# Kernel tuning notes

Measured on AMD Instinct MI355X. Metric: run time of the kernel, lower is better.

The kernel has to match this reference:

```python
import jax, jax.numpy as jnp
import numpy as np

N = 100000
E = 1600000
IN_C, HID_C, OUT_C = 128, 64, 64
LAYERS = 2


def setup_inputs() -> dict:
    key = jax.random.key(0)
    ks = jax.random.split(key, 7)
    x = jax.random.normal(ks[0], (N, IN_C), dtype=jnp.float32)
    edge_index = jax.random.randint(ks[1], (2, E), 0, N, dtype=jnp.int32)
    W_init = jax.random.normal(ks[2], (IN_C, HID_C), dtype=jnp.float32) / np.sqrt(IN_C)
    W_self = jax.random.normal(ks[3], (LAYERS, HID_C, HID_C), dtype=jnp.float32) / np.sqrt(HID_C)
    W_agg = jax.random.normal(ks[4], (LAYERS, HID_C, HID_C), dtype=jnp.float32) / np.sqrt(HID_C)
    b = jnp.zeros((LAYERS, HID_C), dtype=jnp.float32)
    W_out = jax.random.normal(ks[5], (HID_C, OUT_C), dtype=jnp.float32) / np.sqrt(HID_C)
    return {"x": x, "edge_index": edge_index, "W_init": W_init,
            "W_self": W_self, "W_agg": W_agg, "b": b, "W_out": W_out}


def reference(x, edge_index, W_init, W_self, W_agg, b, W_out):
    # edge (dst, src): aggregated_neighbors[edge[0]].append(x[edge[1]])
    dst = edge_index[0]
    src = edge_index[1]
    n = x.shape[0]
    # in-degree for mean aggregation (clamp to 1 for isolated nodes)
    deg = jax.ops.segment_sum(jnp.ones((src.shape[0],), dtype=x.dtype), dst,
                              num_segments=n)
    deg = jnp.maximum(deg, 1.0)[:, None]  # [N,1]
    h = x @ W_init  # initialize: [N, hid]
    for l in range(LAYERS):
        msgs = h[src]  # per-edge gather [E, hid]
        agg = jax.ops.segment_sum(msgs, dst, num_segments=n) / deg  # mean aggregate
        h = jax.nn.relu(agg @ W_agg[l] + h @ W_self[l] + b[l])  # combine
    return h @ W_out  # output: [N, out]
```

## Files before the change

### kernel.cpp

```cpp
#include <hip/hip_runtime.h>
#include <hip/hip_fp16.h>

#define N_NODES 100000
#define E_EDGES 1600000
#define IN_C    128
#define HID_C   64
#define OUT_C   64
#define ROWS    32
#define NBUCK   391
#define BSHIFT  8
#define BNODES  256
#define CAP     5120
#define CHUNK   4096

typedef _Float16 f16x8 __attribute__((ext_vector_type(8)));
typedef float    f32x4 __attribute__((ext_vector_type(4)));
#define MFMA16(a, b, c) __builtin_amdgcn_mfma_f32_16x16x32_f16(a, b, c, 0, 0, 0)

__global__ __launch_bounds__(256) void bin_kernel(const int* __restrict__ ei,
                                                  int* __restrict__ bucket_cursor,
                                                  unsigned int* __restrict__ gbuck) {
    __shared__ int hist[NBUCK];
    __shared__ int resbase[NBUCK];
    __shared__ int cur[NBUCK];
    __shared__ unsigned int pk[CHUNK];
    __shared__ unsigned short bk[CHUNK];
    int tid = threadIdx.x;
    for (int i = tid; i < NBUCK; i += 256) hist[i] = 0;
    __syncthreads();
    int base = blockIdx.x * CHUNK;
    for (int i = tid; i < CHUNK; i += 256) {
        int e = base + i;
        if (e < E_EDGES) {
            int dst = ei[e];
            int src = ei[E_EDGES + e];
            int b = dst >> BSHIFT;
            pk[i] = ((unsigned)(dst & (BNODES - 1)) << 17) | (unsigned)src;
            bk[i] = (unsigned short)b;
            atomicAdd(&hist[b], 1);
        } else bk[i] = 0xFFFF;
    }
    __syncthreads();
    for (int i = tid; i < NBUCK; i += 256) {
        resbase[i] = atomicAdd(&bucket_cursor[i], hist[i]);
        cur[i] = 0;
    }
    __syncthreads();
    for (int i = tid; i < CHUNK; i += 256) {
        if (bk[i] != 0xFFFF) {
            int b = bk[i];
            int slot = resbase[b] + atomicAdd(&cur[b], 1);
            if (slot < CAP) gbuck[(size_t)b * CAP + slot] = pk[i];
        }
    }
}

__global__ __launch_bounds__(512) void scan_buckets(const int* __restrict__ bucket_cursor,
                                                    int* __restrict__ bucket_base) {
    __shared__ int s[512];
    int t = threadIdx.x;
    int v = (t < NBUCK) ? min(bucket_cursor[t], CAP) : 0;
    s[t] = v;
    __syncthreads();
    for (int off = 1; off < 512; off <<= 1) {
        int u = (t >= off) ? s[t - off] : 0;
        __syncthreads();
        s[t] += u;
        __syncthreads();
    }
    if (t < NBUCK) bucket_base[t] = s[t] - v;
}

__global__ __launch_bounds__(256) void build_bucket(const unsigned int* __restrict__ gbuck,
                                                    const int* __restrict__ bucket_cursor,
                                                    const int* __restrict__ bucket_base,
                                                    int* __restrict__ csr,
                                                    int2* __restrict__ rc) {
    __shared__ int lcnt[BNODES];
    __shared__ int lpos[BNODES];
    __shared__ int lcur[BNODES];
    __shared__ int ss[256];
    int t = threadIdx.x;
    int b = blockIdx.x;
    int gnode = b * BNODES;
    int nn = min(BNODES, N_NODES - gnode);
    int ec = min(bucket_cursor[b], CAP);
    int bb = bucket_base[b];
    lcnt[t] = 0; lcur[t] = 0;
    __syncthreads();
    const unsigned int* mybuck = gbuck + (size_t)b * CAP;
    for (int i = t; i < ec; i += 256)
        atomicAdd(&lcnt[mybuck[i] >> 17], 1);
    __syncthreads();
    int c = lcnt[t];
    ss[t] = c;
    __syncthreads();
    for (int off = 1; off < 256; off <<= 1) {
        int u = (t >= off) ? ss[t - off] : 0;
        __syncthreads();
        ss[t] += u;
        __syncthreads();
    }
    int ex = ss[t] - c;
    lpos[t] = ex;
    if (t < nn) rc[gnode + t] = make_int2(bb + ex, c);
    __syncthreads();
    for (int i = t; i < ec; i += 256) {
        unsigned int p = mybuck[i];
        int dl = p >> 17;
        int slot = lpos[dl] + atomicAdd(&lcur[dl], 1);
        csr[bb + slot] = (int)(p & 0x1FFFF);
    }
}

__global__ __launch_bounds__(256) void transpose_weights(const float* __restrict__ Wi,
                                                         const float* __restrict__ Wsf,
                                                         const float* __restrict__ Waf,
                                                         const float* __restrict__ Wo,
                                                         _Float16* __restrict__ wtr) {
    int t = blockIdx.x * 256 + threadIdx.x;
    if (t < 8192) {
        int k = t >> 6, col = t & 63;
        wtr[col * 136 + k] = (_Float16)Wi[t];
    } else if (t < 24576) {
        int u = t - 8192; int l = u >> 13; int v = u & 8191;
        int k = v >> 6, col = v & 63;
        float w = (k < 64) ? Waf[l * 4096 + k * 64 + col] : Wsf[l * 4096 + (k - 64) * 64 + col];
        wtr[8704 + l * 8704 + col * 136 + k] = (_Float16)w;
    } else if (t < 28672) {
        int u = t - 24576; int k = u >> 6, col = u & 63;
        wtr[26112 + col * 72 + k] = (_Float16)Wo[u];
    }
}

template<int K>
__device__ __forceinline__ void mfma_tile(const _Float16* sA, const _Float16* sBt,
                                          int lane, int wave, f32x4 acc[2]) {
    const int LDA = K + 8;
    int r0 = (wave >> 1) * 16;
    int wc = wave & 1;
    int m = lane & 15, kg = lane >> 4;
    acc[0] = (f32x4){0.f, 0.f, 0.f, 0.f};
    acc[1] = (f32x4){0.f, 0.f, 0.f, 0.f};
    #pragma unroll
    for (int ks = 0; ks < K / 32; ++ks) {
        f16x8 a = *(const f16x8*)&sA[(r0 + m) * LDA + 32 * ks + 8 * kg];
        #pragma unroll
        for (int nt = 0; nt < 2; ++nt) {
            f16x8 b = *(const f16x8*)&sBt[(wc * 32 + nt * 16 + m) * LDA + 32 * ks + 8 * kg];
            acc[nt] = MFMA16(a, b, acc[nt]);
        }
    }
}

__global__ __launch_bounds__(256) void init_gemm(const float* __restrict__ x,
                                                 const float4* __restrict__ wtrI,
                                                 __half* __restrict__ h) {
    __shared__ _Float16 sA[ROWS][IN_C + 8];
    __shared__ _Float16 sBt[HID_C][IN_C + 8];
    int tid = threadIdx.x;
    float4* sB4 = (float4*)&sBt[0][0];
    for (int i = tid; i < 1088; i += 256) sB4[i] = wtrI[i];
    int row0 = blockIdx.x * ROWS;
    const float4* x4 = (const float4*)x;
    for (int i = tid; i < ROWS * 32; i += 256) {
        int r = i >> 5, q = i & 31;
        float4 f = x4[(size_t)(row0 + r) * 32 + q];
        __half2 ha = __floats2half2_rn(f.x, f.y), hb = __floats2half2_rn(f.z, f.w);
        uint2 u; u.x = *(unsigned*)&ha; u.y = *(unsigned*)&hb;
        *(uint2*)&sA[r][q * 4] = u;
    }
    __syncthreads();
    int lane = tid & 63, wave = tid >> 6;
    f32x4 acc[2];
    mfma_tile<IN_C>(&sA[0][0], &sBt[0][0], lane, wave, acc);
    int m = lane & 15, rg = lane >> 4;
    int r0 = (wave >> 1) * 16, wc = wave & 1;
    #pragma unroll
    for (int nt = 0; nt < 2; ++nt) {
        int col = wc * 32 + nt * 16 + m;
        #pragma unroll
        for (int i = 0; i < 4; ++i) {
            int row = row0 + r0 + rg * 4 + i;
            h[(size_t)row * HID_C + col] = __float2half(acc[nt][i]);
        }
    }
}

template<bool FINAL>
__global__ __launch_bounds__(256) void fused_layer(const __half* __restrict__ h,
                                                   const int2* __restrict__ rc,
                                                   const int* __restrict__ csr,
                                                   const float4* __restrict__ wtrL,
                                                   const float* __restrict__ bias,
                                                   __half* __restrict__ hout,
                                                   const float4* __restrict__ wtrO,
                                                   float* __restrict__ out) {
    __shared__ _Float16 sA[ROWS][136];
    __shared__ _Float16 sBt[HID_C][136];
    int tid = threadIdx.x;
    float4* sB4 = (float4*)&sBt[0][0];
    for (int i = tid; i < 1088; i += 256) sB4[i] = wtrL[i];
    int row0 = blockIdx.x * ROWS;
    int wave = tid >> 6, lane = tid & 63;
    int g4 = lane >> 4;
    int c16 = lane & 15;
    const uint2* h2u = (const uint2*)h;
    const __half2 hzero = __floats2half2_rn(0.f, 0.f);
    for (int i = 0; i < 8; ++i) {
        int rl = wave * 8 + i;
        int row = row0 + rl;
        int2 rcv = rc[row];
        int start = __builtin_amdgcn_readfirstlane(rcv.x);
        int d     = __builtin_amdgcn_readfirstlane(rcv.y);
        uint2 selfv = h2u[(size_t)row * 16 + c16];
        __half2 p01 = hzero, p23 = hzero;
        int j = 0;
        for (; j + 16 <= d; j += 16) {
            uint2 v[4];
            #pragma unroll
            for (int s = 0; s < 4; ++s) {
                int src = csr[start + j + s * 4 + g4];
                v[s] = h2u[(size_t)src * 16 + c16];
            }
            #pragma unroll
            for (int s = 0; s < 4; ++s) {
                p01 += *(__half2*)&v[s].x;
                p23 += *(__half2*)&v[s].y;
            }
        }
        if (j < d) {
            int dm1 = d - 1;
            #pragma unroll
            for (int s = 0; s < 4; ++s) {
                int e = j + s * 4 + g4;
                bool ok = e < d;
                int src = csr[start + min(e, dm1)];
                uint2 vv = h2u[(size_t)src * 16 + c16];
                unsigned vx = ok ? vv.x : 0u, vy = ok ? vv.y : 0u;
                p01 += *(__half2*)&vx;
                p23 += *(__half2*)&vy;
            }
        }
        unsigned u01 = *(unsigned*)&p01, u23 = *(unsigned*)&p23;
        unsigned o01 = (unsigned)__shfl_xor((int)u01, 16), o23 = (unsigned)__shfl_xor((int)u23, 16);
        p01 += *(__half2*)&o01; p23 += *(__half2*)&o23;
        u01 = *(unsigned*)&p01; u23 = *(unsigned*)&p23;
        o01 = (unsigned)__shfl_xor((int)u01, 32); o23 = (unsigned)__shfl_xor((int)u23, 32);
        p01 += *(__half2*)&o01; p23 += *(__half2*)&o23;
        if (lane < 16) {
            __half2 hinv = __float2half2_rn(1.f / fmaxf((float)d, 1.f));
            p01 *= hinv; p23 *= hinv;
            uint2 agg2; agg2.x = *(unsigned*)&p01; agg2.y = *(unsigned*)&p23;
            *(uint2*)&sA[rl][4 * c16]      = agg2;
            *(uint2*)&sA[rl][64 + 4 * c16] = selfv;
        }
    }
    __syncthreads();
    f32x4 acc[2];
    mfma_tile<128>(&sA[0][0], &sBt[0][0], lane, wave, acc);
    int m = lane & 15, rg = lane >> 4;
    int r0 = (wave >> 1) * 16, wc = wave & 1;
    if (!FINAL) {
        #pragma unroll
        for (int nt = 0; nt < 2; ++nt) {
            int col = wc * 32 + nt * 16 + m;
            float bv = bias[col];
            #pragma unroll
            for (int i = 0; i < 4; ++i) {
                int row = row0 + r0 + rg * 4 + i;
                hout[(size_t)row * HID_C + col] = __float2half(fmaxf(acc[nt][i] + bv, 0.f));
            }
        }
    } else {
        __syncthreads();
        _Float16* sA72 = &sA[0][0];
        #pragma unroll
        for (int nt = 0; nt < 2; ++nt) {
            int col = wc * 32 + nt * 16 + m;
            float bv = bias[col];
            #pragma unroll
            for (int i = 0; i < 4; ++i) {
                int rl = r0 + rg * 4 + i;
                sA72[rl * 72 + col] = (_Float16)fmaxf(acc[nt][i] + bv, 0.f);
            }
        }
        for (int i = tid; i < 576; i += 256) sB4[i] = wtrO[i];
        __syncthreads();
        f32x4 acc2[2];
        mfma_tile<64>(&sA[0][0], &sBt[0][0], lane, wave, acc2);
        #pragma unroll
        for (int nt = 0; nt < 2; ++nt) {
            int col = wc * 32 + nt * 16 + m;
            #pragma unroll
            for (int i = 0; i < 4; ++i) {
                int row = row0 + r0 + rg * 4 + i;
                out[(size_t)row * OUT_C + col] = acc2[nt][i];
            }
        }
    }
}

extern "C" void kernel_launch(void* const* d_in, const int* in_sizes, int n_in,
                              void* d_out, int out_size, void* d_ws, size_t ws_size,
                              hipStream_t stream) {
    const float* x      = (const float*)d_in[0];
    const int*   ei     = (const int*)  d_in[1];
    const float* W_init = (const float*)d_in[2];
    const float* W_self = (const float*)d_in[3];
    const float* W_agg  = (const float*)d_in[4];
    const float* b      = (const float*)d_in[5];
    const float* W_out  = (const float*)d_in[6];
    float* out = (float*)d_out;

    char* ws = (char*)d_ws;
    const size_t KB = 1 << 10;
    int*      bucket_cursor = (int*)(ws + 0);
    int*      bucket_base   = (int*)(ws + 2 * KB);
    int2*     rc            = (int2*)(ws + 4 * KB);
    int*      csr           = (int*)(ws + 1024 * KB);
    _Float16* wtr           = (_Float16*)(ws + 7424 * KB);
    unsigned* gbuck         = (unsigned*)(ws + 8192 * KB);
    __half*   hA            = (__half*)(ws + 18432 * KB);
    __half*   hB            = (__half*)(ws + 32768 * KB);

    const float4* wtrI  = (const float4*)(wtr);
    const float4* wtrL0 = (const float4*)(wtr + 8704);
    const float4* wtrL1 = (const float4*)(wtr + 17408);
    const float4* wtrO  = (const float4*)(wtr + 26112);

    transpose_weights<<<112, 256, 0, stream>>>(W_init, W_self, W_agg, W_out, wtr);

    hipMemsetAsync(bucket_cursor, 0, NBUCK * sizeof(int), stream);
    bin_kernel<<<(E_EDGES + CHUNK - 1) / CHUNK, 256, 0, stream>>>(ei, bucket_cursor, gbuck);
    scan_buckets<<<1, 512, 0, stream>>>(bucket_cursor, bucket_base);
    build_bucket<<<NBUCK, 256, 0, stream>>>(gbuck, bucket_cursor, bucket_base, csr, rc);

    const int GB = N_NODES / ROWS;

    init_gemm<<<GB, 256, 0, stream>>>(x, wtrI, hA);

    fused_layer<false><<<GB, 256, 0, stream>>>(hA, rc, csr, wtrL0, b + 0 * HID_C, hB,
                                               wtrO, out);
    fused_layer<true><<<GB, 256, 0, stream>>>(hB, rc, csr, wtrL1, b + 1 * HID_C, hA,
                                              wtrO, out);
}
```

Measured before the change: 168.4 us.

## Merge preprocessing kernels and stage CSR indices in LDS for batched gather

Combines binning with the weight transpose in one launch, and folds the bucket scan into the CSR build, which runs in the same launch as the init GEMM. This cuts six launches to two. The fused layer now preloads each block's CSR index range and self rows into shared memory, then gathers eight rows at once with unrolled chunks to raise memory-level parallelism. Costs are redundant per-block scans, higher register pressure, and a capped index buffer (IDXMAX) that clamps edges for blocks with unusually many edges.

Result: faster. 144.0 us (-14.5%).

```diff
diff --git a/kernel.cpp b/kernel.cpp
--- a/kernel.cpp
+++ b/kernel.cpp
@@ -12,126 +12,78 @@
 #define BNODES  256
 #define CAP     5120
 #define CHUNK   4096
+#define NB_BINCH 391
+#define NB_TR   112
+#define IDXCAP  1632
+#define IDXMAX  1568
 
 typedef _Float16 f16x8 __attribute__((ext_vector_type(8)));
 typedef float    f32x4 __attribute__((ext_vector_type(4)));
 #define MFMA16(a, b, c) __builtin_amdgcn_mfma_f32_16x16x32_f16(a, b, c, 0, 0, 0)
 
-__global__ __launch_bounds__(256) void bin_kernel(const int* __restrict__ ei,
-                                                  int* __restrict__ bucket_cursor,
-                                                  unsigned int* __restrict__ gbuck) {
-    __shared__ int hist[NBUCK];
-    __shared__ int resbase[NBUCK];
-    __shared__ int cur[NBUCK];
-    __shared__ unsigned int pk[CHUNK];
-    __shared__ unsigned short bk[CHUNK];
+struct BinS {
+    int hist[NBUCK]; int resbase[NBUCK]; int cur[NBUCK];
+    unsigned pk[CHUNK]; unsigned short bk[CHUNK];
+};
+
+__global__ __launch_bounds__(256) void k1_bin_tr(const int* __restrict__ ei,
+                                                 int* __restrict__ bucket_cursor,
+                                                 unsigned* __restrict__ gbuck,
+                                                 const float* __restrict__ Wi,
+                                                 const float* __restrict__ Wsf,
+                                                 const float* __restrict__ Waf,
+                                                 const float* __restrict__ Wo,
+                                                 _Float16* __restrict__ wtr) {
+    __shared__ BinS S;
     int tid = threadIdx.x;
-    for (int i = tid; i < NBUCK; i += 256) hist[i] = 0;
-    __syncthreads();
-    int base = blockIdx.x * CHUNK;
-    for (int i = tid; i < CHUNK; i += 256) {
-        int e = base + i;
-        if (e < E_EDGES) {
-            int dst = ei[e];
-            int src = ei[E_EDGES + e];
-            int b = dst >> BSHIFT;
-            pk[i] = ((unsigned)(dst & (BNODES - 1)) << 17) | (unsigned)src;
-            bk[i] = (unsigned short)b;
-            atomicAdd(&hist[b], 1);
-        } else bk[i] = 0xFFFF;
-    }
-    __syncthreads();
-    for (int i = tid; i < NBUCK; i += 256) {
-        resbase[i] = atomicAdd(&bucket_cursor[i], hist[i]);
-        cur[i] = 0;
-    }
-    __syncthreads();
-    for (int i = tid; i < CHUNK; i += 256) {
-        if (bk[i] != 0xFFFF) {
-            int b = bk[i];
-            int slot = resbase[b] + atomicAdd(&cur[b], 1);
-            if (slot < CAP) gbuck[(size_t)b * CAP + slot] = pk[i];
-        }
-    }
-}
-
-__global__ __launch_bounds__(512) void scan_buckets(const int* __restrict__ bucket_cursor,
-                                                    int* __restrict__ bucket_base) {
-    __shared__ int s[512];
-    int t = threadIdx.x;
-    int v = (t < NBUCK) ? min(bucket_cursor[t], CAP) : 0;
-    s[t] = v;
-    __syncthreads();
-    for (int off = 1; off < 512; off <<= 1) {
-        int u = (t >= off) ? s[t - off] : 0;
-        __syncthreads();
-        s[t] += u;
-        __syncthreads();
-    }
-    if (t < NBUCK) bucket_base[t] = s[t] - v;
-}
-
-__global__ __launch_bounds__(256) void build_bucket(const unsigned int* __restrict__ gbuck,
-                                                    const int* __restrict__ bucket_cursor,
-                                                    const int* __restrict__ bucket_base,
-                                                    int* __restrict__ csr,
-                                                    int2* __restrict__ rc) {
-    __shared__ int lcnt[BNODES];
-    __shared__ int lpos[BNODES];
-    __shared__ int lcur[BNODES];
-    __shared__ int ss[256];
-    int t = threadIdx.x;
-    int b = blockIdx.x;
-    int gnode = b * BNODES;
-    int nn = min(BNODES, N_NODES - gnode);
-    int ec = min(bucket_cursor[b], CAP);
-    int bb = bucket_base[b];
-    lcnt[t] = 0; lcur[t] = 0;
-    __syncthreads();
-    const unsigned int* mybuck = gbuck + (size_t)b * CAP;
-    for (int i = t; i < ec; i += 256)
-        atomicAdd(&lcnt[mybuck[i] >> 17], 1);
-    __syncthreads();
-    int c = lcnt[t];
-    ss[t] = c;
-    __syncthreads();
-    for (int off = 1; off < 256; off <<= 1) {
-        int u = (t >= off) ? ss[t - off] : 0;
-        __syncthreads();
-        ss[t] += u;
-        __syncthreads();
-    }
-    int ex = ss[t] - c;
-    lpos[t] = ex;
-    if (t < nn) rc[gnode + t] = make_int2(bb + ex, c);
-    __syncthreads();
-    for (int i = t; i < ec; i += 256) {
-        unsigned int p = mybuck[i];
-        int dl = p >> 17;
-        int slot = lpos[dl] + atomicAdd(&lcur[dl], 1);
-        csr[bb + slot] = (int)(p & 0x1FFFF);
-    }
-}
-
-__global__ __launch_bounds__(256) void transpose_weights(const float* __restrict__ Wi,
-                                                         const float* __restrict__ Wsf,
-                                                         const float* __restrict__ Waf,
-                                                         const float* __restrict__ Wo,
-                                                         _Float16* __restrict__ wtr) {
-    int t = blockIdx.x * 256 + threadIdx.x;
-    if (t < 8192) {
-        int k = t >> 6, col = t & 63;
-        wtr[col * 136 + k] = (_Float16)Wi[t];
-    } else if (t < 24576) {
-        int u = t - 8192; int l = u >> 13; int v = u & 8191;
-        int k = v >> 6, col = v & 63;
-        float w = (k < 64) ? Waf[l * 4096 + k * 64 + col] : Wsf[l * 4096 + (k - 64) * 64 + col];
-        wtr[8704 + l * 8704 + col * 136 + k] = (_Float16)w;
-    } else if (t < 28672) {
-        int u = t - 24576; int k = u >> 6, col = u & 63;
-        wtr[26112 + col * 72 + k] = (_Float16)Wo[u];
-    }
-}
+    if (blockIdx.x < NB_BINCH) {
+        for (int i = tid; i < NBUCK; i += 256) S.hist[i] = 0;
+        __syncthreads();
+        int base = blockIdx.x * CHUNK;
+        for (int i = tid; i < CHUNK; i += 256) {
+            int e = base + i;
+            if (e < E_EDGES) {
+                int dst = ei[e];
+                int src = ei[E_EDGES + e];
+                int b = dst >> BSHIFT;
+                S.pk[i] = ((unsigned)(dst & (BNODES - 1)) << 17) | (unsigned)src;
+                S.bk[i] = (unsigned short)b;
+                atomicAdd(&S.hist[b], 1);
+            } else S.bk[i] = 0xFFFF;
+        }
+        __syncthreads();
+        for (int i = tid; i < NBUCK; i += 256) {
+            S.resbase[i] = atomicAdd(&bucket_cursor[i], S.hist[i]);
+            S.cur[i] = 0;
+        }
+        __syncthreads();
+        for (int i = tid; i < CHUNK; i += 256) {
+            if (S.bk[i] != 0xFFFF) {
+                int b = S.bk[i];
+                int slot = S.resbase[b] + atomicAdd(&S.cur[b], 1);
+                if (slot < CAP) gbuck[(size_t)b * CAP + slot] = S.pk[i];
+            }
+        }
+    } else {
+        int t = (blockIdx.x - NB_BINCH) * 256 + tid;
+        if (t < 8192) {
+            int k = t >> 6, col = t & 63;
+            wtr[col * 136 + k] = (_Float16)Wi[t];
+        } else if (t < 24576) {
+            int u = t - 8192; int l = u >> 13; int v = u & 8191;
+            int k = v >> 6, col = v & 63;
+            float w = (k < 64) ? Waf[l * 4096 + k * 64 + col] : Wsf[l * 4096 + (k - 64) * 64 + col];
+            wtr[8704 + l * 8704 + col * 136 + k] = (_Float16)w;
+        } else if (t < 28672) {
+            int u = t - 24576; int k = u >> 6, col = u & 63;
+            wtr[26112 + col * 72 + k] = (_Float16)Wo[u];
+        }
+    }
+}
+
+struct InitS { _Float16 sA[ROWS][IN_C + 8]; _Float16 sBt[HID_C][IN_C + 8]; };
+struct BuildS { int lcnt[BNODES]; int lpos[BNODES]; int lcur[BNODES]; int s[2][512]; };
+union K2S { InitS ini; BuildS bld; };
 
 template<int K>
 __device__ __forceinline__ void mfma_tile(const _Float16* sA, const _Float16* sBt,
@@ -153,39 +105,105 @@
     }
 }
 
-__global__ __launch_bounds__(256) void init_gemm(const float* __restrict__ x,
-                                                 const float4* __restrict__ wtrI,
-                                                 __half* __restrict__ h) {
-    __shared__ _Float16 sA[ROWS][IN_C + 8];
-    __shared__ _Float16 sBt[HID_C][IN_C + 8];
-    int tid = threadIdx.x;
-    float4* sB4 = (float4*)&sBt[0][0];
-    for (int i = tid; i < 1088; i += 256) sB4[i] = wtrI[i];
-    int row0 = blockIdx.x * ROWS;
-    const float4* x4 = (const float4*)x;
-    for (int i = tid; i < ROWS * 32; i += 256) {
-        int r = i >> 5, q = i & 31;
-        float4 f = x4[(size_t)(row0 + r) * 32 + q];
-        __half2 ha = __floats2half2_rn(f.x, f.y), hb = __floats2half2_rn(f.z, f.w);
-        uint2 u; u.x = *(unsigned*)&ha; u.y = *(unsigned*)&hb;
-        *(uint2*)&sA[r][q * 4] = u;
-    }
-    __syncthreads();
-    int lane = tid & 63, wave = tid >> 6;
-    f32x4 acc[2];
-    mfma_tile<IN_C>(&sA[0][0], &sBt[0][0], lane, wave, acc);
-    int m = lane & 15, rg = lane >> 4;
-    int r0 = (wave >> 1) * 16, wc = wave & 1;
-    #pragma unroll
-    for (int nt = 0; nt < 2; ++nt) {
-        int col = wc * 32 + nt * 16 + m;
-        #pragma unroll
-        for (int i = 0; i < 4; ++i) {
-            int row = row0 + r0 + rg * 4 + i;
-            h[(size_t)row * HID_C + col] = __float2half(acc[nt][i]);
-        }
-    }
-}
+__global__ __launch_bounds__(256) void k2_build_init(const unsigned* __restrict__ gbuck,
+                                                     const int* __restrict__ bucket_cursor,
+                                                     int* __restrict__ csr,
+                                                     int2* __restrict__ rc,
+                                                     const float* __restrict__ x,
+                                                     const float4* __restrict__ wtrI,
+                                                     __half* __restrict__ h) {
+    __shared__ K2S U;
+    int t = threadIdx.x;
+    if (blockIdx.x < NBUCK) {
+        BuildS& S = U.bld;
+        int b = blockIdx.x;
+        int v0 = (t < NBUCK) ? min(bucket_cursor[t], CAP) : 0;
+        int v1 = (t + 256 < NBUCK) ? min(bucket_cursor[t + 256], CAP) : 0;
+        S.s[0][t] = v0; S.s[0][t + 256] = v1;
+        S.lcnt[t] = 0; S.lcur[t] = 0;
+        __syncthreads();
+        int p = 0;
+        for (int off = 1; off < 512; off <<= 1) {
+            int a0 = S.s[p][t]       + ((t >= off)       ? S.s[p][t - off] : 0);
+            int a1 = S.s[p][t + 256] + ((t + 256 >= off) ? S.s[p][t + 256 - off] : 0);
+            S.s[p ^ 1][t] = a0; S.s[p ^ 1][t + 256] = a1;
+            __syncthreads();
+            p ^= 1;
+        }
+        int bb = (b == 0) ? 0 : S.s[p][b - 1];
+        int ec = min(bucket_cursor[b], CAP);
+        int gnode = b * BNODES;
+        int nn = min(BNODES, N_NODES - gnode);
+        const unsigned* mybuck = gbuck + (size_t)b * CAP;
+        __syncthreads();
+        for (int i = t; i < ec; i += 256) atomicAdd(&S.lcnt[mybuck[i] >> 17], 1);
+        __syncthreads();
+        int c = S.lcnt[t];
+        S.s[0][t] = c;
+        __syncthreads();
+        int q = 0;
+        for (int off = 1; off < 256; off <<= 1) {
+            int a0 = S.s[q][t] + ((t >= off) ? S.s[q][t - off] : 0);
+            S.s[q ^ 1][t] = a0;
+            __syncthreads();
+            q ^= 1;
+        }
+        int ex = S.s[q][t] - c;
+        S.lpos[t] = ex;
+        if (t < nn) rc[gnode + t] = make_int2(bb + ex, c);
+        __syncthreads();
+        for (int i = t; i < ec; i += 256) {
+            unsigned pkt = mybuck[i];
+            int dl = pkt >> 17;
+            int slot = S.lpos[dl] + atomicAdd(&S.lcur[dl], 1);
+            csr[bb + slot] = (int)(pkt & 0x1FFFF);
+        }
+    } else {
+        InitS& S = U.ini;
+        int row0 = (blockIdx.x - NBUCK) * ROWS;
+        float4* sB4 = (float4*)&S.sBt[0][0];
+        for (int i = t; i < 1088; i += 256) sB4[i] = wtrI[i];
+        const float4* x4 = (const float4*)x;
+        for (int i = t; i < ROWS * 32; i += 256) {
+            int r = i >> 5, qq = i & 31;
+            float4 f = x4[(size_t)(row0 + r) * 32 + qq];
+            __half2 ha = __floats2half2_rn(f.x, f.y), hb = __floats2half2_rn(f.z, f.w);
+            uint2 u; u.x = *(unsigned*)&ha; u.y = *(unsigned*)&hb;
+            *(uint2*)&S.sA[r][qq * 4] = u;
+        }
+        __syncthreads();
+        int lane = t & 63, wave = t >> 6;
+        f32x4 acc[2];
+        mfma_tile<IN_C>(&S.sA[0][0], &S.sBt[0][0], lane, wave, acc);
+        int m = lane & 15, rg = lane >> 4;
+        int r0 = (wave >> 1) * 16, wc = wave & 1;
+        #pragma unroll
+        for (int nt = 0; nt < 2; ++nt) {
+            int col = wc * 32 + nt * 16 + m;
+            #pragma unroll
+            for (int i = 0; i < 4; ++i) {
+                int row = row0 + r0 + rg * 4 + i;
+                h[(size_t)row * HID_C + col] = __float2half(acc[nt][i]);
+            }
+        }
+    }
+}
+
+#define GCHUNK(r, JB, CLAMP)                                                    \
+    {                                                                           \
+        _Pragma("unroll")                                                       \
+        for (int s = 0; s < 4; ++s) {                                           \
+            int ee = (JB) + s * 4 + g4;                                         \
+            int a = sl[r] + ee;                                                 \
+            if (CLAMP) a = min(a, IDXCAP - 1);                                  \
+            int src = sIdx[a];                                                  \
+            uint2 vv = h2u[(size_t)src * 16 + c16];                             \
+            bool ok = ee < dd[r];                                               \
+            unsigned vx = ok ? vv.x : 0u, vy = ok ? vv.y : 0u;                  \
+            p01[r] += *(__half2*)&vx;                                           \
+            p23[r] += *(__half2*)&vy;                                           \
+        }                                                                       \
+    }
 
 template<bool FINAL>
 __global__ __launch_bounds__(256) void fused_layer(const __half* __restrict__ h,
@@ -198,65 +216,75 @@
                                                    float* __restrict__ out) {
     __shared__ _Float16 sA[ROWS][136];
     __shared__ _Float16 sBt[HID_C][136];
+    __shared__ int sIdx[IDXCAP];
+    __shared__ int2 sRC[ROWS];
     int tid = threadIdx.x;
     float4* sB4 = (float4*)&sBt[0][0];
     for (int i = tid; i < 1088; i += 256) sB4[i] = wtrL[i];
     int row0 = blockIdx.x * ROWS;
+    const uint2* h2u = (const uint2*)h;
+
+    if (tid < 32) sRC[tid] = rc[row0 + tid];
+    int2 rcF = rc[row0];
+    int2 rcL = rc[row0 + 31];
+    int e0 = __builtin_amdgcn_readfirstlane(rcF.x);
+    int e1 = __builtin_amdgcn_readfirstlane(rcL.x) + __builtin_amdgcn_readfirstlane(rcL.y);
+    int Lc = min(e1 - e0, IDXMAX);
+    for (int i = tid; i < Lc; i += 256) sIdx[i] = csr[e0 + i];
+    if (tid < 64) sIdx[min(Lc + tid, IDXCAP - 1)] = 0;
+    for (int i = tid; i < 512; i += 256) {
+        int r = i >> 4, qq = i & 15;
+        *(uint2*)&sA[r][64 + qq * 4] = h2u[(size_t)(row0 + r) * 16 + qq];
+    }
+    __syncthreads();
+
     int wave = tid >> 6, lane = tid & 63;
     int g4 = lane >> 4;
     int c16 = lane & 15;
-    const uint2* h2u = (const uint2*)h;
+    int sl[8], dd[8];
+    #pragma unroll
+    for (int r = 0; r < 8; ++r) {
+        int2 v = sRC[wave * 8 + r];
+        sl[r] = min(__builtin_amdgcn_readfirstlane(v.x) - e0, IDXMAX);
+        dd[r] = __builtin_amdgcn_readfirstlane(v.y);
+    }
     const __half2 hzero = __floats2half2_rn(0.f, 0.f);
-    for (int i = 0; i < 8; ++i) {
-        int rl = wave * 8 + i;
-        int row = row0 + rl;
-        int2 rcv = rc[row];
-        int start = __builtin_amdgcn_readfirstlane(rcv.x);
-        int d     = __builtin_amdgcn_readfirstlane(rcv.y);
-        uint2 selfv = h2u[(size_t)row * 16 + c16];
-        __half2 p01 = hzero, p23 = hzero;
-        int j = 0;
-        for (; j + 16 <= d; j += 16) {
-            uint2 v[4];
-            #pragma unroll
-            for (int s = 0; s < 4; ++s) {
-                int src = csr[start + j + s * 4 + g4];
-                v[s] = h2u[(size_t)src * 16 + c16];
-            }
-            #pragma unroll
-            for (int s = 0; s < 4; ++s) {
-                p01 += *(__half2*)&v[s].x;
-                p23 += *(__half2*)&v[s].y;
-            }
-        }
-        if (j < d) {
-            int dm1 = d - 1;
-            #pragma unroll
-            for (int s = 0; s < 4; ++s) {
-                int e = j + s * 4 + g4;
-                bool ok = e < d;
-                int src = csr[start + min(e, dm1)];
-                uint2 vv = h2u[(size_t)src * 16 + c16];
-                unsigned vx = ok ? vv.x : 0u, vy = ok ? vv.y : 0u;
-                p01 += *(__half2*)&vx;
-                p23 += *(__half2*)&vy;
-            }
-        }
-        unsigned u01 = *(unsigned*)&p01, u23 = *(unsigned*)&p23;
-        unsigned o01 = (unsigned)__shfl_xor((int)u01, 16), o23 = (unsigned)__shfl_xor((int)u23, 16);
-        p01 += *(__half2*)&o01; p23 += *(__half2*)&o23;
-        u01 = *(unsigned*)&p01; u23 = *(unsigned*)&p23;
-        o01 = (unsigned)__shfl_xor((int)u01, 32); o23 = (unsigned)__shfl_xor((int)u23, 32);
-        p01 += *(__half2*)&o01; p23 += *(__half2*)&o23;
+    __half2 p01[8], p23[8];
+    #pragma unroll
+    for (int r = 0; r < 8; ++r) { p01[r] = hzero; p23[r] = hzero; }
+
+    #pragma unroll
+    for (int r = 0; r < 8; ++r) GCHUNK(r, 0, false)
+    #pragma unroll
+    for (int r = 0; r < 8; ++r) GCHUNK(r, 16, false)
+    int dmax = dd[0];
+    #pragma unroll
+    for (int r = 1; r < 8; ++r) dmax = max(dmax, dd[r]);
+    if (dmax > 32) {
+        #pragma unroll
+        for (int r = 0; r < 8; ++r)
+            for (int j = 32; j < dd[r]; j += 16) GCHUNK(r, j, true)
+    }
+
+    #pragma unroll
+    for (int r = 0; r < 8; ++r) {
+        unsigned u01 = *(unsigned*)&p01[r], u23 = *(unsigned*)&p23[r];
+        unsigned o01 = (unsigned)__shfl_xor((int)u01, 16);
+        unsigned o23 = (unsigned)__shfl_xor((int)u23, 16);
+        p01[r] += *(__half2*)&o01; p23[r] += *(__half2*)&o23;
+        u01 = *(unsigned*)&p01[r]; u23 = *(unsigned*)&p23[r];
+        o01 = (unsigned)__shfl_xor((int)u01, 32);
+        o23 = (unsigned)__shfl_xor((int)u23, 32);
+        p01[r] += *(__half2*)&o01; p23[r] += *(__half2*)&o23;
         if (lane < 16) {
-            __half2 hinv = __float2half2_rn(1.f / fmaxf((float)d, 1.f));
-            p01 *= hinv; p23 *= hinv;
-            uint2 agg2; agg2.x = *(unsigned*)&p01; agg2.y = *(unsigned*)&p23;
-            *(uint2*)&sA[rl][4 * c16]      = agg2;
-            *(uint2*)&sA[rl][64 + 4 * c16] = selfv;
+            __half2 hinv = __float2half2_rn(1.f / fmaxf((float)dd[r], 1.f));
+            __half2 q01 = p01[r] * hinv, q23 = p23[r] * hinv;
+            uint2 agg2; agg2.x = *(unsigned*)&q01; agg2.y = *(unsigned*)&q23;
+            *(uint2*)&sA[wave * 8 + r][4 * c16] = agg2;
         }
     }
     __syncthreads();
+
     f32x4 acc[2];
     mfma_tile<128>(&sA[0][0], &sBt[0][0], lane, wave, acc);
     int m = lane & 15, rg = lane >> 4;
@@ -316,7 +344,6 @@
     char* ws = (char*)d_ws;
     const size_t KB = 1 << 10;
     int*      bucket_cursor = (int*)(ws + 0);
-    int*      bucket_base   = (int*)(ws + 2 * KB);
     int2*     rc            = (int2*)(ws + 4 * KB);
     int*      csr           = (int*)(ws + 1024 * KB);
     _Float16* wtr           = (_Float16*)(ws + 7424 * KB);
@@ -329,17 +356,12 @@
     const float4* wtrL1 = (const float4*)(wtr + 17408);
     const float4* wtrO  = (const float4*)(wtr + 26112);
 
-    transpose_weights<<<112, 256, 0, stream>>>(W_init, W_self, W_agg, W_out, wtr);
-
     hipMemsetAsync(bucket_cursor, 0, NBUCK * sizeof(int), stream);
-    bin_kernel<<<(E_EDGES + CHUNK - 1) / CHUNK, 256, 0, stream>>>(ei, bucket_cursor, gbuck);
-    scan_buckets<<<1, 512, 0, stream>>>(bucket_cursor, bucket_base);
-    build_bucket<<<NBUCK, 256, 0, stream>>>(gbuck, bucket_cursor, bucket_base, csr, rc);
-
+    k1_bin_tr<<<NB_BINCH + NB_TR, 256, 0, stream>>>(ei, bucket_cursor, gbuck,
+                                                    W_init, W_self, W_agg, W_out, wtr);
+    k2_build_init<<<NBUCK + N_NODES / ROWS, 256, 0, stream>>>(gbuck, bucket_cursor, csr, rc,
+                                                              x, wtrI, hA);
     const int GB = N_NODES / ROWS;
-
-    init_gemm<<<GB, 256, 0, stream>>>(x, wtrI, hA);
-
     fused_layer<false><<<GB, 256, 0, stream>>>(hA, rc, csr, wtrL0, b + 0 * HID_C, hB,
                                                wtrO, out);
     fused_layer<true><<<GB, 256, 0, stream>>>(hB, rc, csr, wtrL1, b + 1 * HID_C, hA,
```
